# Performance work log

Measured on AMD Instinct MI355X. Metric: run time of the kernel, lower is better.

The kernel has to match this reference:

```python
import jax, jax.numpy as jnp
import numpy as np

B, T_SEQ, STATE, DIM_IN, DIM_K, DIM_V, LAYER = 8, 2048, 128, 1024, 64, 64, 4
T = T_SEQ + 2 * STATE  # 2304
LAMBDA_INIT = 0.8 - 0.6 * float(np.exp(-0.3 * LAYER))
NEG = -1e30


def setup_inputs() -> dict:
    key = jax.random.key(0)
    ks = jax.random.split(key, 20)
    def w(k, shape):
        return jax.random.normal(k, shape, dtype=jnp.float32) * 0.02
    inp = {"x": jax.random.normal(ks[0], (B, T, DIM_IN), dtype=jnp.float32)}
    # projection weights stored as (in, out) so y = x @ W
    inp["Wq"] = w(ks[1], (DIM_IN, 2 * DIM_K)); inp["Wk"] = w(ks[2], (DIM_IN, 2 * DIM_K)); inp["Wv"] = w(ks[3], (DIM_IN, 2 * DIM_V))
    inp["Wq_ss"] = w(ks[4], (DIM_IN, 2 * DIM_K)); inp["Wk_ss"] = w(ks[5], (DIM_IN, 2 * DIM_K)); inp["Wv_ss"] = w(ks[6], (DIM_IN, 2 * DIM_V))
    inp["Wq_se"] = w(ks[7], (DIM_IN, 2 * DIM_K)); inp["Wk_se"] = w(ks[8], (DIM_IN, 2 * DIM_K)); inp["Wv_se"] = w(ks[9], (DIM_IN, 2 * DIM_V))
    # layernorm params (torch defaults: ones/zeros)
    inp["g_in"] = jnp.ones((DIM_IN,), jnp.float32); inp["b_in"] = jnp.zeros((DIM_IN,), jnp.float32)
    inp["g_ss"] = jnp.ones((DIM_IN,), jnp.float32); inp["b_ss"] = jnp.zeros((DIM_IN,), jnp.float32)
    inp["g_se"] = jnp.ones((DIM_IN,), jnp.float32); inp["b_se"] = jnp.zeros((DIM_IN,), jnp.float32)
    inp["g_out"] = jnp.ones((2 * DIM_V,), jnp.float32); inp["b_out"] = jnp.zeros((2 * DIM_V,), jnp.float32)
    # lambda gate params
    inp["lq1"] = jax.random.normal(ks[10], (1, DIM_K), jnp.float32)
    inp["lq2"] = jax.random.normal(ks[11], (1, DIM_K), jnp.float32)
    inp["lk1"] = jax.random.normal(ks[12], (DIM_K, 1), jnp.float32)
    inp["lk2"] = jax.random.normal(ks[13], (DIM_K, 1), jnp.float32)
    return inp


def _ln(z, g, b, eps=1e-5):
    m = jnp.mean(z, axis=-1, keepdims=True)
    v = jnp.mean((z - m) ** 2, axis=-1, keepdims=True)
    return (z - m) * jax.lax.rsqrt(v + eps) * g + b


def reference(x, Wq, Wk, Wv, Wq_ss, Wk_ss, Wv_ss, Wq_se, Wk_se, Wv_se,
              g_in, b_in, g_ss, b_ss, g_se, b_se, g_out, b_out,
              lq1, lq2, lk1, lk2):
    # extract_state: split off state tokens at both ends
    xs, xm, xe = x[:, :STATE], x[:, STATE:-STATE], x[:, -STATE:]
    xm = _ln(xm, g_in, b_in)
    xs = _ln(xs, g_ss, b_ss)
    xe = _ln(xe, g_se, b_se)
    q = jnp.concatenate([xs @ Wq_ss, xm @ Wq, xe @ Wq_se], axis=1)  # (B,T,2K)
    k = jnp.concatenate([xs @ Wk_ss, xm @ Wk, xe @ Wk_se], axis=1)
    v = jnp.concatenate([xs @ Wv_ss, xm @ Wv, xe @ Wv_se], axis=1)  # (B,T,2V)
    q1, q2 = q[..., :DIM_K], q[..., DIM_K:]
    k1, k2 = k[..., :DIM_K], k[..., DIM_K:]
    scale = 1.0 / np.sqrt(DIM_K)
    t = q.shape[1]
    causal = jnp.triu(jnp.full((t, t), NEG, dtype=q.dtype), k=1)  # (T,T)
    s1 = jnp.einsum('btd,bsd->bts', q1, k1) * scale + causal
    s2 = jnp.einsum('btd,bsd->bts', q2, k2) * scale + causal
    a1 = jax.nn.softmax(s1, axis=-1)
    a2 = jax.nn.softmax(s2, axis=-1)
    o1 = jnp.einsum('bts,bsd->btd', a1, v)
    o2 = jnp.einsum('bts,bsd->btd', a2, v)
    lam = (jnp.exp(lq1 @ lk1) - jnp.exp(lq2 @ lk2))[0, 0] + LAMBDA_INIT
    att = o1 - lam * o2
    return _ln(att, g_out, b_out)
```

## Files before the change

### kernel.cpp

```cpp
#include <hip/hip_runtime.h>
#include <hip/hip_bf16.h>
#include <stdint.h>

#define B_ 8
#define T_ 2304
#define DIN 1024
#define LAMBDA_INIT_F 0.6192834728526788f

typedef __bf16 bf16x8 __attribute__((ext_vector_type(8)));
typedef float f32x4 __attribute__((ext_vector_type(4)));

__device__ __forceinline__ unsigned short f2bf(float f) {
    union { float f; unsigned int u; } v; v.f = f;
    unsigned int u = v.u;
    unsigned int r = (u + 0x7FFFu + ((u >> 16) & 1u)) >> 16;
    return (unsigned short)r;
}

__device__ __forceinline__ unsigned int pack2bf(float lo, float hi) {
    return ((unsigned int)f2bf(hi) << 16) | (unsigned int)f2bf(lo);
}

__global__ __launch_bounds__(256) void k_wtrans(
    const float* w0, const float* w1, const float* w2,
    const float* w3, const float* w4, const float* w5,
    const float* w6, const float* w7, const float* w8,
    unsigned short* __restrict__ wt)
{
    __shared__ float tile[64][65];
    int bx = blockIdx.x;
    int mat = bx >> 5;
    int tl = bx & 31;
    int tx = tl & 15;
    int ty = tl >> 4;
    const float* srcs[9] = {w0, w1, w2, w3, w4, w5, w6, w7, w8};
    const float* src = srcs[mat];
    int k0 = tx * 64, c0 = ty * 64;
    int t = threadIdx.x;
    int r = t >> 2, cg = (t & 3) << 4;
    const float* p = src + (size_t)(k0 + r) * 128 + c0 + cg;
#pragma unroll
    for (int i = 0; i < 4; ++i) {
        float4 v = *(const float4*)(p + i * 4);
        tile[r][cg + i * 4 + 0] = v.x;
        tile[r][cg + i * 4 + 1] = v.y;
        tile[r][cg + i * 4 + 2] = v.z;
        tile[r][cg + i * 4 + 3] = v.w;
    }
    __syncthreads();
    int seg = mat / 3, m = mat % 3;
    int crow = seg * 384 + m * 128 + c0 + r;
    unsigned short* dst = wt + (size_t)crow * 1024 + k0 + cg;
    __align__(16) unsigned short ob[16];
#pragma unroll
    for (int i = 0; i < 16; ++i) ob[i] = f2bf(tile[cg + i][r]);
    *(uint4*)(dst) = *(const uint4*)(ob);
    *(uint4*)(dst + 8) = *(const uint4*)(ob + 8);
}

__global__ __launch_bounds__(256) void k_ln(
    const float* __restrict__ x,
    const float* __restrict__ g_in, const float* __restrict__ b_in,
    const float* __restrict__ g_ss, const float* __restrict__ b_ss,
    const float* __restrict__ g_se, const float* __restrict__ b_se,
    unsigned short* __restrict__ xbf)
{
    int row = (blockIdx.x << 2) + (threadIdx.x >> 6);
    int l = threadIdx.x & 63;
    int t = row % T_;
    const float* gv; const float* bv;
    if (t < 128)       { gv = g_ss; bv = b_ss; }
    else if (t < 2176) { gv = g_in; bv = b_in; }
    else               { gv = g_se; bv = b_se; }
    const float* xp = x + (size_t)row * DIN + l * 4;
    float4 v0 = *(const float4*)(xp);
    float4 v1 = *(const float4*)(xp + 256);
    float4 v2 = *(const float4*)(xp + 512);
    float4 v3 = *(const float4*)(xp + 768);
    float s  = v0.x + v0.y + v0.z + v0.w + v1.x + v1.y + v1.z + v1.w
             + v2.x + v2.y + v2.z + v2.w + v3.x + v3.y + v3.z + v3.w;
    float s2 = v0.x*v0.x + v0.y*v0.y + v0.z*v0.z + v0.w*v0.w
             + v1.x*v1.x + v1.y*v1.y + v1.z*v1.z + v1.w*v1.w
             + v2.x*v2.x + v2.y*v2.y + v2.z*v2.z + v2.w*v2.w
             + v3.x*v3.x + v3.y*v3.y + v3.z*v3.z + v3.w*v3.w;
#pragma unroll
    for (int off = 1; off <= 32; off <<= 1) {
        s  += __shfl_xor(s,  off);
        s2 += __shfl_xor(s2, off);
    }
    float mean = s * (1.f / 1024.f);
    float rstd = rsqrtf(s2 * (1.f / 1024.f) - mean * mean + 1e-5f);
    unsigned short* op = xbf + (size_t)row * DIN + l * 4;
    const float* gp = gv + l * 4;
    const float* bp = bv + l * 4;
#pragma unroll
    for (int k = 0; k < 4; ++k) {
        float4 vv = (k == 0) ? v0 : (k == 1) ? v1 : (k == 2) ? v2 : v3;
        float4 gk = *(const float4*)(gp + k * 256);
        float4 bk = *(const float4*)(bp + k * 256);
        uint2 o;
        o.x = pack2bf((vv.x - mean) * rstd * gk.x + bk.x,
                      (vv.y - mean) * rstd * gk.y + bk.y);
        o.y = pack2bf((vv.z - mean) * rstd * gk.z + bk.z,
                      (vv.w - mean) * rstd * gk.w + bk.w);
        *(uint2*)(op + k * 256) = o;
    }
}

__global__ __launch_bounds__(512, 4) void k_proj2(
    const unsigned short* __restrict__ xbf,
    const unsigned short* __restrict__ wt,
    unsigned short* __restrict__ qo,
    unsigned short* __restrict__ ko,
    unsigned short* __restrict__ vto)
{
    __shared__ __align__(16) char smem[81920];

    int bid = blockIdx.x;
    int mt = bid >> 1, ch = bid & 1;
    int bb = mt / 18, tt = mt % 18;
    int seg = (tt == 0) ? 0 : ((tt < 17) ? 1 : 2);
    size_t arow0 = (size_t)mt * 128;
    int ncol0 = ch * 192;
    int wrow0 = seg * 384 + ncol0;

    int tid = threadIdx.x;
    int w = tid >> 6, l = tid & 63;
    int wr = w >> 2, wc = w & 3;
    int g4 = l >> 4, cr = l & 15;

    int rA0 = tid >> 3, cS = (tid & 7) << 4;
    const char* srcA0 = (const char*)xbf + (arow0 + rA0) * 2048 + cS;
    const char* srcA1 = srcA0 + (size_t)64 * 2048;
    int dA0 = rA0 * 128 + (cS ^ ((rA0 & 7) << 4));
    int dA1 = dA0 + 64 * 128;
    const char* srcW0 = (const char*)wt + (size_t)(wrow0 + rA0) * 2048 + cS;
    const char* srcW1 = srcW0 + (size_t)64 * 2048;
    const char* srcW2 = srcW0 + (size_t)128 * 2048;
    int dW0 = dA0, dW1 = dA0 + 64 * 128, dW2 = dA0 + 128 * 128;

    {
        uint4 a0 = *(const uint4*)srcA0;
        uint4 a1 = *(const uint4*)srcA1;
        uint4 w0 = *(const uint4*)srcW0;
        uint4 w1 = *(const uint4*)srcW1;
        uint4 w2 = *(const uint4*)srcW2;
        *(uint4*)(smem + dA0) = a0;
        *(uint4*)(smem + dA1) = a1;
        *(uint4*)(smem + 32768 + dW0) = w0;
        *(uint4*)(smem + 32768 + dW1) = w1;
        *(uint4*)(smem + 32768 + dW2) = w2;
    }
    __syncthreads();

    f32x4 acc[4][3] = {};
    for (int ks = 0; ks < 16; ++ks) {
        bool pf = (ks < 15);
        uint4 pa0, pa1, pw0, pw1, pw2;
        if (pf) {
            size_t o = (size_t)(ks + 1) * 128;
            pa0 = *(const uint4*)(srcA0 + o);
            pa1 = *(const uint4*)(srcA1 + o);
            pw0 = *(const uint4*)(srcW0 + o);
            pw1 = *(const uint4*)(srcW1 + o);
            pw2 = *(const uint4*)(srcW2 + o);
        }
        const char* Ab = smem + (ks & 1) * 16384;
        const char* Wb = smem + 32768 + (ks & 1) * 24576;
        __builtin_amdgcn_s_setprio(1);
#pragma unroll
        for (int kk = 0; kk < 2; ++kk) {
            int kb = kk * 64 + g4 * 16;
            bf16x8 af[4];
#pragma unroll
            for (int r4 = 0; r4 < 4; ++r4) {
                int rr = wr * 64 + r4 * 16 + cr;
                af[r4] = *(const bf16x8*)(Ab + rr * 128 + (kb ^ ((rr & 7) << 4)));
            }
            bf16x8 bfr[3];
#pragma unroll
            for (int nt = 0; nt < 3; ++nt) {
                int c = wc * 48 + nt * 16 + cr;
                bfr[nt] = *(const bf16x8*)(Wb + c * 128 + (kb ^ ((c & 7) << 4)));
            }
#pragma unroll
            for (int r4 = 0; r4 < 4; ++r4)
#pragma unroll
                for (int nt = 0; nt < 3; ++nt)
                    acc[r4][nt] = __builtin_amdgcn_mfma_f32_16x16x32_bf16(af[r4], bfr[nt], acc[r4][nt], 0, 0, 0);
        }
        __builtin_amdgcn_s_setprio(0);
        __syncthreads();
        if (pf) {
            char* An = smem + ((ks + 1) & 1) * 16384;
            char* Wn = smem + 32768 + ((ks + 1) & 1) * 24576;
            *(uint4*)(An + dA0) = pa0;
            *(uint4*)(An + dA1) = pa1;
            *(uint4*)(Wn + dW0) = pw0;
            *(uint4*)(Wn + dW1) = pw1;
            *(uint4*)(Wn + dW2) = pw2;
        }
        __syncthreads();
    }

#pragma unroll
    for (int r4 = 0; r4 < 4; ++r4) {
        size_t grow = arow0 + wr * 64 + r4 * 16 + g4 * 4;
#pragma unroll
        for (int nt = 0; nt < 3; ++nt) {
            int c = ncol0 + wc * 48 + nt * 16 + cr;
            f32x4 a = acc[r4][nt];
            if (c < 128) {
#pragma unroll
                for (int g = 0; g < 4; ++g)
                    qo[(grow + g) * 128 + c] = f2bf(a[g]);
            } else if (c < 256) {
#pragma unroll
                for (int g = 0; g < 4; ++g)
                    ko[(grow + g) * 128 + (c - 128)] = f2bf(a[g]);
            } else {
                int cv = c - 256;
                int trow = tt * 128 + wr * 64 + r4 * 16 + g4 * 4;
                uint2 o;
                o.x = pack2bf(a[0], a[1]);
                o.y = pack2bf(a[2], a[3]);
                *(uint2*)(vto + ((size_t)bb * 128 + cv) * T_ + trow) = o;
            }
        }
    }
}

__global__ __launch_bounds__(512, 2) void k_attn(
    const unsigned short* __restrict__ qp_,
    const unsigned short* __restrict__ kp_,
    const unsigned short* __restrict__ vp_,
    const float* __restrict__ lq1, const float* __restrict__ lq2,
    const float* __restrict__ lk1, const float* __restrict__ lk2,
    const float* __restrict__ g_out, const float* __restrict__ b_out,
    float* __restrict__ out)
{
    __shared__ __align__(16) char smem[69632];

    int bid = blockIdx.x;
    int j = 35 - (bid >> 3);
    int b = bid & 7;
    int t0 = j * 64;
    int tid = threadIdx.x;
    int w8 = tid >> 6;
    int qg = w8 & 3;
    int p  = w8 >> 2;
    int l = tid & 63;
    int g4 = l >> 4, q = l & 15;
    int q_g = t0 + qg * 16 + q;
    int grp = tid >> 8;
    int u = tid & 255;

    int rK = u >> 2, cK = (u & 3) << 6;
    const char* srcK0 = (const char*)(kp_ + ((size_t)b * T_ + rK) * 128) + cK;
    int rV = u >> 1, cV = (u & 1) << 6;
    const char* srcV0 = (const char*)(vp_ + ((size_t)b * 128 + rV) * T_) + cV;
    int swK = (rK & 7) << 4;
    char* KwB = smem + grp * 16384 + rK * 256;
    int oko0 = (cK +  0) ^ swK, oko1 = (cK + 16) ^ swK;
    int oko2 = (cK + 32) ^ swK, oko3 = (cK + 48) ^ swK;
    int swV = (rV & 7) << 4;
    char* VwB = smem + 32768 + grp * 16384 + rV * 128;
    int ovo0 = (cV +  0) ^ swV, ovo1 = (cV + 16) ^ swV;
    int ovo2 = (cV + 32) ^ swV, ovo3 = (cV + 48) ^ swV;

    bf16x8 qf[2][2];
#pragma unroll
    for (int br = 0; br < 2; ++br)
#pragma unroll
        for (int h = 0; h < 2; ++h)
            qf[br][h] = *(const bf16x8*)(qp_ + ((size_t)b * T_ + q_g) * 128 + br * 64 + h * 32 + g4 * 8);

    if (grp <= j) {
        const char* sK = srcK0 + (size_t)grp * 16384;
        uint4 ka0 = *(const uint4*)(sK);
        uint4 ka1 = *(const uint4*)(sK + 16);
        uint4 ka2 = *(const uint4*)(sK + 32);
        uint4 ka3 = *(const uint4*)(sK + 48);
        const char* sV = srcV0 + (size_t)grp * 128;
        uint4 va0 = *(const uint4*)(sV);
        uint4 va1 = *(const uint4*)(sV + 16);
        uint4 va2 = *(const uint4*)(sV + 32);
        uint4 va3 = *(const uint4*)(sV + 48);
        *(uint4*)(KwB + oko0) = ka0;
        *(uint4*)(KwB + oko1) = ka1;
        *(uint4*)(KwB + oko2) = ka2;
        *(uint4*)(KwB + oko3) = ka3;
        *(uint4*)(VwB + ovo0) = va0;
        *(uint4*)(VwB + ovo1) = va1;
        *(uint4*)(VwB + ovo2) = va2;
        *(uint4*)(VwB + ovo3) = va3;
    }
    __syncthreads();

    float mrun[2] = {-1e30f, -1e30f};
    float lrun[2] = {0.f, 0.f};
    f32x4 oacc[2][8] = {};
    const char* Kb = smem + p * 16384;
    const char* Vb = smem + 32768 + p * 16384;

    int nph = (j >> 1) + 1;
    for (int t = 0; t < nph; ++t) {
        int pf = 2 * (t + 1) + grp;
        bool pfv = (pf <= j);
        uint4 ka0, ka1, ka2, ka3, va0, va1, va2, va3;
        if (pfv) {
            const char* sK = srcK0 + (size_t)pf * 16384;
            ka0 = *(const uint4*)(sK);
            ka1 = *(const uint4*)(sK + 16);
            ka2 = *(const uint4*)(sK + 32);
            ka3 = *(const uint4*)(sK + 48);
            const char* sV = srcV0 + (size_t)pf * 128;
            va0 = *(const uint4*)(sV);
            va1 = *(const uint4*)(sV + 16);
            va2 = *(const uint4*)(sV + 32);
            va3 = *(const uint4*)(sV + 48);
        }

        int kt = 2 * t + p;
        if (kt <= j) {
            bool diag = (kt == j);
            unsigned int pk[2][4][2];
#pragma unroll
            for (int br = 0; br < 2; ++br) {
                f32x4 s[4] = {};
                __builtin_amdgcn_s_setprio(1);
#pragma unroll
                for (int h = 0; h < 2; ++h) {
#pragma unroll
                    for (int t4 = 0; t4 < 4; ++t4) {
                        int rk = t4 * 16 + q;
                        bf16x8 kf = *(const bf16x8*)(Kb + rk * 256 + ((br * 128 + h * 64 + g4 * 16) ^ ((rk & 7) << 4)));
                        s[t4] = __builtin_amdgcn_mfma_f32_16x16x32_bf16(kf, qf[br][h], s[t4], 0, 0, 0);
                    }
                }
                __builtin_amdgcn_s_setprio(0);
                float sv[16];
                float mx = -1e30f;
#pragma unroll
                for (int t4 = 0; t4 < 4; ++t4)
#pragma unroll
                    for (int r = 0; r < 4; ++r) {
                        float v = s[t4][r] * 0.125f;
                        if (diag) {
                            int kv_g = kt * 64 + t4 * 16 + g4 * 4 + r;
                            if (kv_g > q_g) v = -1e30f;
                        }
                        sv[t4 * 4 + r] = v;
                        mx = fmaxf(mx, v);
                    }
                mx = fmaxf(mx, __shfl_xor(mx, 16));
                mx = fmaxf(mx, __shfl_xor(mx, 32));
                float mn;
                if (__all(mx <= mrun[br] + 8.f)) {
                    mn = mrun[br];
                } else {
                    mn = fmaxf(mrun[br], mx);
                    float sf = __expf(mrun[br] - mn);
                    mrun[br] = mn;
                    lrun[br] *= sf;
#pragma unroll
                    for (int dblk = 0; dblk < 8; ++dblk)
#pragma unroll
                        for (int r = 0; r < 4; ++r)
                            oacc[br][dblk][r] *= sf;
                }
                float pr[16];
                float rs = 0.f;
#pragma unroll
                for (int i = 0; i < 16; ++i) {
                    pr[i] = __expf(sv[i] - mn);
                    rs += pr[i];
                }
                rs += __shfl_xor(rs, 16);
                rs += __shfl_xor(rs, 32);
                lrun[br] += rs;
#pragma unroll
                for (int t4 = 0; t4 < 4; ++t4) {
                    pk[br][t4][0] = pack2bf(pr[t4 * 4 + 0], pr[t4 * 4 + 1]);
                    pk[br][t4][1] = pack2bf(pr[t4 * 4 + 2], pr[t4 * 4 + 3]);
                }
            }
#pragma unroll
            for (int h = 0; h < 2; ++h) {
                bf16x8 pb[2];
                int s0 = q + (((g4 * 2) & 3) << 4);
                int s1 = q + (((g4 * 2 + 1) & 3) << 4);
                int sel = g4 >> 1;
#pragma unroll
                for (int br = 0; br < 2; ++br) {
                    unsigned int m0a = (unsigned int)__shfl((int)pk[br][2 * h][0], s0);
                    unsigned int m0b = (unsigned int)__shfl((int)pk[br][2 * h + 1][0], s0);
                    unsigned int m1a = (unsigned int)__shfl((int)pk[br][2 * h][1], s0);
                    unsigned int m1b = (unsigned int)__shfl((int)pk[br][2 * h + 1][1], s0);
                    unsigned int m2a = (unsigned int)__shfl((int)pk[br][2 * h][0], s1);
                    unsigned int m2b = (unsigned int)__shfl((int)pk[br][2 * h + 1][0], s1);
                    unsigned int m3a = (unsigned int)__shfl((int)pk[br][2 * h][1], s1);
                    unsigned int m3b = (unsigned int)__shfl((int)pk[br][2 * h + 1][1], s1);
                    union { unsigned int uu[4]; bf16x8 v; } pu;
                    pu.uu[0] = sel ? m0b : m0a;
                    pu.uu[1] = sel ? m1b : m1a;
                    pu.uu[2] = sel ? m2b : m2a;
                    pu.uu[3] = sel ? m3b : m3a;
                    pb[br] = pu.v;
                }
                __builtin_amdgcn_s_setprio(1);
#pragma unroll
                for (int dblk = 0; dblk < 8; ++dblk) {
                    int rv = dblk * 16 + q;
                    bf16x8 vf = *(const bf16x8*)(Vb + rv * 128 + ((h * 64 + g4 * 16) ^ ((rv & 7) << 4)));
                    oacc[0][dblk] = __builtin_amdgcn_mfma_f32_16x16x32_bf16(vf, pb[0], oacc[0][dblk], 0, 0, 0);
                    oacc[1][dblk] = __builtin_amdgcn_mfma_f32_16x16x32_bf16(vf, pb[1], oacc[1][dblk], 0, 0, 0);
                }
                __builtin_amdgcn_s_setprio(0);
            }
        }
        __syncthreads();
        if (pfv) {
            *(uint4*)(KwB + oko0) = ka0;
            *(uint4*)(KwB + oko1) = ka1;
            *(uint4*)(KwB + oko2) = ka2;
            *(uint4*)(KwB + oko3) = ka3;
            *(uint4*)(VwB + ovo0) = va0;
            *(uint4*)(VwB + ovo1) = va1;
            *(uint4*)(VwB + ovo2) = va2;
            *(uint4*)(VwB + ovo3) = va3;
        }
        __syncthreads();
    }

    float* Osh = (float*)smem;
    float* Msh = (float*)(smem + 65536);
    if (p == 1) {
        int base = qg * 4096 + l;
#pragma unroll
        for (int br = 0; br < 2; ++br)
#pragma unroll
            for (int dblk = 0; dblk < 8; ++dblk)
#pragma unroll
                for (int r = 0; r < 4; ++r)
                    Osh[base + (br * 32 + dblk * 4 + r) * 64] = oacc[br][dblk][r];
        float4 ml;
        ml.x = mrun[0]; ml.y = lrun[0]; ml.z = mrun[1]; ml.w = lrun[1];
        *(float4*)(Msh + (qg * 64 + l) * 4) = ml;
    }
    __syncthreads();
    if (p == 0) {
        float4 ml = *(const float4*)(Msh + (qg * 64 + l) * 4);
        float m1v[2] = {ml.x, ml.z}, l1v[2] = {ml.y, ml.w};
        float lfin[2], a0[2], a1[2];
#pragma unroll
        for (int br = 0; br < 2; ++br) {
            float mstar = fmaxf(mrun[br], m1v[br]);
            a0[br] = __expf(mrun[br] - mstar);
            a1[br] = __expf(m1v[br] - mstar);
            lfin[br] = a0[br] * lrun[br] + a1[br] * l1v[br];
        }
        int base = qg * 4096 + l;
#pragma unroll
        for (int br = 0; br < 2; ++br)
#pragma unroll
            for (int dblk = 0; dblk < 8; ++dblk)
#pragma unroll
                for (int r = 0; r < 4; ++r)
                    oacc[br][dblk][r] = a0[br] * oacc[br][dblk][r]
                        + a1[br] * Osh[base + (br * 32 + dblk * 4 + r) * 64];

        float pa = lq1[l] * lk1[l];
        float pb2 = lq2[l] * lk2[l];
#pragma unroll
        for (int off = 32; off >= 1; off >>= 1) {
            pa += __shfl_xor(pa, off);
            pb2 += __shfl_xor(pb2, off);
        }
        float lam = __expf(pa) - __expf(pb2) + LAMBDA_INIT_F;

        float att[8][4];
        float sm = 0.f;
        float inv1 = 1.f / lfin[0], inv2 = 1.f / lfin[1];
#pragma unroll
        for (int dblk = 0; dblk < 8; ++dblk)
#pragma unroll
            for (int r = 0; r < 4; ++r) {
                float a = oacc[0][dblk][r] * inv1 - lam * (oacc[1][dblk][r] * inv2);
                att[dblk][r] = a;
                sm += a;
            }
        sm += __shfl_xor(sm, 16);
        sm += __shfl_xor(sm, 32);
        float mean = sm * (1.f / 128.f);
        float sv2 = 0.f;
#pragma unroll
        for (int dblk = 0; dblk < 8; ++dblk)
#pragma unroll
            for (int r = 0; r < 4; ++r) {
                float d = att[dblk][r] - mean;
                sv2 += d * d;
            }
        sv2 += __shfl_xor(sv2, 16);
        sv2 += __shfl_xor(sv2, 32);
        float rstd = rsqrtf(sv2 * (1.f / 128.f) + 1e-5f);

        float* orow = out + ((size_t)b * T_ + q_g) * 128;
#pragma unroll
        for (int dblk = 0; dblk < 8; ++dblk) {
            int d0 = dblk * 16 + g4 * 4;
            float4 o;
            o.x = (att[dblk][0] - mean) * rstd * g_out[d0 + 0] + b_out[d0 + 0];
            o.y = (att[dblk][1] - mean) * rstd * g_out[d0 + 1] + b_out[d0 + 1];
            o.z = (att[dblk][2] - mean) * rstd * g_out[d0 + 2] + b_out[d0 + 2];
            o.w = (att[dblk][3] - mean) * rstd * g_out[d0 + 3] + b_out[d0 + 3];
            *(float4*)(orow + d0) = o;
        }
    }
}

extern "C" void kernel_launch(void* const* d_in, const int* in_sizes, int n_in,
                              void* d_out, int out_size, void* d_ws, size_t ws_size,
                              hipStream_t stream) {
    (void)in_sizes; (void)n_in; (void)out_size; (void)ws_size;
    const float* x = (const float*)d_in[0];
    char* ws = (char*)d_ws;
    unsigned short* wt  = (unsigned short*)ws;
    unsigned short* xbf = (unsigned short*)(ws + 2359296);
    unsigned short* qo  = (unsigned short*)(ws + 40108032);
    unsigned short* ko  = (unsigned short*)(ws + 44826624);
    unsigned short* vto = (unsigned short*)(ws + 49545216);

    hipLaunchKernelGGL(k_wtrans, dim3(288), dim3(256), 0, stream,
        (const float*)d_in[4], (const float*)d_in[5], (const float*)d_in[6],
        (const float*)d_in[1], (const float*)d_in[2], (const float*)d_in[3],
        (const float*)d_in[7], (const float*)d_in[8], (const float*)d_in[9], wt);

    hipLaunchKernelGGL(k_ln, dim3(4608), dim3(256), 0, stream,
        x,
        (const float*)d_in[10], (const float*)d_in[11],
        (const float*)d_in[12], (const float*)d_in[13],
        (const float*)d_in[14], (const float*)d_in[15],
        xbf);

    hipLaunchKernelGGL(k_proj2, dim3(288), dim3(512), 0, stream,
        xbf, wt, qo, ko, vto);

    hipLaunchKernelGGL(k_attn, dim3(288), dim3(512), 0, stream,
        qo, ko, vto,
        (const float*)d_in[18], (const float*)d_in[19],
        (const float*)d_in[20], (const float*)d_in[21],
        (const float*)d_in[16], (const float*)d_in[17],
        (float*)d_out);
}
```

Measured before the change: 131.2 us.

## Split long causal attention rows into KV chunks with a separate merge kernel

Query tiles with many causal KV tiles are split into up to three chunks of 12 KV tiles, so the attention grid grows from 288 to 576 blocks with more even work per block. Chunked tiles write bf16 partial outputs together with running max and sum to workspace, and a new merge kernel combines them, applies the lambda difference and the output layernorm. The cost is an extra kernel launch, extra global traffic for the partials, and bf16 rounding of the unnormalized partial accumulators. The partial buffers reuse the workspace region that held xbf.

```diff
diff --git a/kernel.cpp b/kernel.cpp
--- a/kernel.cpp
+++ b/kernel.cpp
@@ -19,6 +19,11 @@
 
 __device__ __forceinline__ unsigned int pack2bf(float lo, float hi) {
     return ((unsigned int)f2bf(hi) << 16) | (unsigned int)f2bf(lo);
+}
+
+__device__ __forceinline__ float bf2f(unsigned short u) {
+    union { unsigned int u; float f; } v; v.u = ((unsigned int)u) << 16;
+    return v.f;
 }
 
 __global__ __launch_bounds__(256) void k_wtrans(
@@ -237,14 +242,24 @@
     const float* __restrict__ lq1, const float* __restrict__ lq2,
     const float* __restrict__ lk1, const float* __restrict__ lk2,
     const float* __restrict__ g_out, const float* __restrict__ b_out,
+    unsigned short* __restrict__ opart,
+    float* __restrict__ mlpart,
     float* __restrict__ out)
 {
     __shared__ __align__(16) char smem[69632];
 
     int bid = blockIdx.x;
-    int j = 35 - (bid >> 3);
     int b = bid & 7;
+    int u = 71 - (bid >> 3);
+    int j, ci;
+    if (u < 12)      { j = u; ci = 0; }
+    else if (u < 36) { int v = u - 12; j = 12 + (v >> 1); ci = v & 1; }
+    else             { int v = u - 36; j = 24 + v / 3; ci = v % 3; }
+    int nch = (j + 12) / 12;
+    int c0 = ci * 12;
+    int ntile = min(12, j + 1 - c0);
     int t0 = j * 64;
+
     int tid = threadIdx.x;
     int w8 = tid >> 6;
     int qg = w8 & 3;
@@ -253,11 +268,11 @@
     int g4 = l >> 4, q = l & 15;
     int q_g = t0 + qg * 16 + q;
     int grp = tid >> 8;
-    int u = tid & 255;
-
-    int rK = u >> 2, cK = (u & 3) << 6;
+    int uu = tid & 255;
+
+    int rK = uu >> 2, cK = (uu & 3) << 6;
     const char* srcK0 = (const char*)(kp_ + ((size_t)b * T_ + rK) * 128) + cK;
-    int rV = u >> 1, cV = (u & 1) << 6;
+    int rV = uu >> 1, cV = (uu & 1) << 6;
     const char* srcV0 = (const char*)(vp_ + ((size_t)b * 128 + rV) * T_) + cV;
     int swK = (rK & 7) << 4;
     char* KwB = smem + grp * 16384 + rK * 256;
@@ -275,13 +290,13 @@
         for (int h = 0; h < 2; ++h)
             qf[br][h] = *(const bf16x8*)(qp_ + ((size_t)b * T_ + q_g) * 128 + br * 64 + h * 32 + g4 * 8);
 
-    if (grp <= j) {
-        const char* sK = srcK0 + (size_t)grp * 16384;
+    if (grp < ntile) {
+        const char* sK = srcK0 + (size_t)(c0 + grp) * 16384;
         uint4 ka0 = *(const uint4*)(sK);
         uint4 ka1 = *(const uint4*)(sK + 16);
         uint4 ka2 = *(const uint4*)(sK + 32);
         uint4 ka3 = *(const uint4*)(sK + 48);
-        const char* sV = srcV0 + (size_t)grp * 128;
+        const char* sV = srcV0 + (size_t)(c0 + grp) * 128;
         uint4 va0 = *(const uint4*)(sV);
         uint4 va1 = *(const uint4*)(sV + 16);
         uint4 va2 = *(const uint4*)(sV + 32);
@@ -303,26 +318,27 @@
     const char* Kb = smem + p * 16384;
     const char* Vb = smem + 32768 + p * 16384;
 
-    int nph = (j >> 1) + 1;
+    int nph = (ntile + 1) >> 1;
     for (int t = 0; t < nph; ++t) {
-        int pf = 2 * (t + 1) + grp;
-        bool pfv = (pf <= j);
+        int lpf = 2 * (t + 1) + grp;
+        bool pfv = (lpf < ntile);
         uint4 ka0, ka1, ka2, ka3, va0, va1, va2, va3;
         if (pfv) {
-            const char* sK = srcK0 + (size_t)pf * 16384;
+            const char* sK = srcK0 + (size_t)(c0 + lpf) * 16384;
             ka0 = *(const uint4*)(sK);
             ka1 = *(const uint4*)(sK + 16);
             ka2 = *(const uint4*)(sK + 32);
             ka3 = *(const uint4*)(sK + 48);
-            const char* sV = srcV0 + (size_t)pf * 128;
+            const char* sV = srcV0 + (size_t)(c0 + lpf) * 128;
             va0 = *(const uint4*)(sV);
             va1 = *(const uint4*)(sV + 16);
             va2 = *(const uint4*)(sV + 32);
             va3 = *(const uint4*)(sV + 48);
         }
 
-        int kt = 2 * t + p;
-        if (kt <= j) {
+        int lt = 2 * t + p;
+        if (lt < ntile) {
+            int kt = c0 + lt;
             bool diag = (kt == j);
             unsigned int pk[2][4][2];
 #pragma unroll
@@ -401,11 +417,11 @@
                     unsigned int m2b = (unsigned int)__shfl((int)pk[br][2 * h + 1][0], s1);
                     unsigned int m3a = (unsigned int)__shfl((int)pk[br][2 * h][1], s1);
                     unsigned int m3b = (unsigned int)__shfl((int)pk[br][2 * h + 1][1], s1);
-                    union { unsigned int uu[4]; bf16x8 v; } pu;
-                    pu.uu[0] = sel ? m0b : m0a;
-                    pu.uu[1] = sel ? m1b : m1a;
-                    pu.uu[2] = sel ? m2b : m2a;
-                    pu.uu[3] = sel ? m3b : m3a;
+                    union { unsigned int uv[4]; bf16x8 v; } pu;
+                    pu.uv[0] = sel ? m0b : m0a;
+                    pu.uv[1] = sel ? m1b : m1a;
+                    pu.uv[2] = sel ? m2b : m2a;
+                    pu.uv[3] = sel ? m3b : m3a;
                     pb[br] = pu.v;
                 }
                 __builtin_amdgcn_s_setprio(1);
@@ -452,70 +468,189 @@
     if (p == 0) {
         float4 ml = *(const float4*)(Msh + (qg * 64 + l) * 4);
         float m1v[2] = {ml.x, ml.z}, l1v[2] = {ml.y, ml.w};
-        float lfin[2], a0[2], a1[2];
+        float lfin[2], mst[2];
 #pragma unroll
         for (int br = 0; br < 2; ++br) {
             float mstar = fmaxf(mrun[br], m1v[br]);
-            a0[br] = __expf(mrun[br] - mstar);
-            a1[br] = __expf(m1v[br] - mstar);
-            lfin[br] = a0[br] * lrun[br] + a1[br] * l1v[br];
-        }
-        int base = qg * 4096 + l;
-#pragma unroll
-        for (int br = 0; br < 2; ++br)
+            float a0 = __expf(mrun[br] - mstar);
+            float a1 = __expf(m1v[br] - mstar);
+            lfin[br] = a0 * lrun[br] + a1 * l1v[br];
+            mst[br] = mstar;
+            int base = qg * 4096 + l;
 #pragma unroll
             for (int dblk = 0; dblk < 8; ++dblk)
 #pragma unroll
                 for (int r = 0; r < 4; ++r)
-                    oacc[br][dblk][r] = a0[br] * oacc[br][dblk][r]
-                        + a1[br] * Osh[base + (br * 32 + dblk * 4 + r) * 64];
-
-        float pa = lq1[l] * lk1[l];
-        float pb2 = lq2[l] * lk2[l];
-#pragma unroll
-        for (int off = 32; off >= 1; off >>= 1) {
-            pa += __shfl_xor(pa, off);
-            pb2 += __shfl_xor(pb2, off);
-        }
-        float lam = __expf(pa) - __expf(pb2) + LAMBDA_INIT_F;
-
-        float att[8][4];
-        float sm = 0.f;
-        float inv1 = 1.f / lfin[0], inv2 = 1.f / lfin[1];
-#pragma unroll
-        for (int dblk = 0; dblk < 8; ++dblk)
-#pragma unroll
-            for (int r = 0; r < 4; ++r) {
-                float a = oacc[0][dblk][r] * inv1 - lam * (oacc[1][dblk][r] * inv2);
-                att[dblk][r] = a;
-                sm += a;
-            }
-        sm += __shfl_xor(sm, 16);
-        sm += __shfl_xor(sm, 32);
-        float mean = sm * (1.f / 128.f);
-        float sv2 = 0.f;
-#pragma unroll
-        for (int dblk = 0; dblk < 8; ++dblk)
-#pragma unroll
-            for (int r = 0; r < 4; ++r) {
-                float d = att[dblk][r] - mean;
-                sv2 += d * d;
-            }
-        sv2 += __shfl_xor(sv2, 16);
-        sv2 += __shfl_xor(sv2, 32);
-        float rstd = rsqrtf(sv2 * (1.f / 128.f) + 1e-5f);
-
-        float* orow = out + ((size_t)b * T_ + q_g) * 128;
-#pragma unroll
-        for (int dblk = 0; dblk < 8; ++dblk) {
-            int d0 = dblk * 16 + g4 * 4;
-            float4 o;
-            o.x = (att[dblk][0] - mean) * rstd * g_out[d0 + 0] + b_out[d0 + 0];
-            o.y = (att[dblk][1] - mean) * rstd * g_out[d0 + 1] + b_out[d0 + 1];
-            o.z = (att[dblk][2] - mean) * rstd * g_out[d0 + 2] + b_out[d0 + 2];
-            o.w = (att[dblk][3] - mean) * rstd * g_out[d0 + 3] + b_out[d0 + 3];
-            *(float4*)(orow + d0) = o;
-        }
+                    oacc[br][dblk][r] = a0 * oacc[br][dblk][r]
+                        + a1 * Osh[base + (br * 32 + dblk * 4 + r) * 64];
+        }
+
+        int row = qg * 16 + q;
+        if (nch == 1) {
+            float pa = lq1[l] * lk1[l];
+            float pb2 = lq2[l] * lk2[l];
+#pragma unroll
+            for (int off = 32; off >= 1; off >>= 1) {
+                pa += __shfl_xor(pa, off);
+                pb2 += __shfl_xor(pb2, off);
+            }
+            float lam = __expf(pa) - __expf(pb2) + LAMBDA_INIT_F;
+
+            float att[8][4];
+            float sm = 0.f;
+            float inv1 = 1.f / lfin[0], inv2 = 1.f / lfin[1];
+#pragma unroll
+            for (int dblk = 0; dblk < 8; ++dblk)
+#pragma unroll
+                for (int r = 0; r < 4; ++r) {
+                    float a = oacc[0][dblk][r] * inv1 - lam * (oacc[1][dblk][r] * inv2);
+                    att[dblk][r] = a;
+                    sm += a;
+                }
+            sm += __shfl_xor(sm, 16);
+            sm += __shfl_xor(sm, 32);
+            float mean = sm * (1.f / 128.f);
+            float sv2 = 0.f;
+#pragma unroll
+            for (int dblk = 0; dblk < 8; ++dblk)
+#pragma unroll
+                for (int r = 0; r < 4; ++r) {
+                    float d = att[dblk][r] - mean;
+                    sv2 += d * d;
+                }
+            sv2 += __shfl_xor(sv2, 16);
+            sv2 += __shfl_xor(sv2, 32);
+            float rstd = rsqrtf(sv2 * (1.f / 128.f) + 1e-5f);
+
+            float* orow = out + ((size_t)b * T_ + q_g) * 128;
+#pragma unroll
+            for (int dblk = 0; dblk < 8; ++dblk) {
+                int d0 = dblk * 16 + g4 * 4;
+                float4 o;
+                o.x = (att[dblk][0] - mean) * rstd * g_out[d0 + 0] + b_out[d0 + 0];
+                o.y = (att[dblk][1] - mean) * rstd * g_out[d0 + 1] + b_out[d0 + 1];
+                o.z = (att[dblk][2] - mean) * rstd * g_out[d0 + 2] + b_out[d0 + 2];
+                o.w = (att[dblk][3] - mean) * rstd * g_out[d0 + 3] + b_out[d0 + 3];
+                *(float4*)(orow + d0) = o;
+            }
+        } else {
+            int slot = (b * 36 + j) * 3 + ci;
+            char* ob = (char*)opart + (size_t)slot * 32768;
+#pragma unroll
+            for (int br = 0; br < 2; ++br) {
+#pragma unroll
+                for (int dblk = 0; dblk < 8; ++dblk) {
+                    uint2 o;
+                    o.x = pack2bf(oacc[br][dblk][0], oacc[br][dblk][1]);
+                    o.y = pack2bf(oacc[br][dblk][2], oacc[br][dblk][3]);
+                    *(uint2*)(ob + br * 16384 + row * 256 + (dblk * 16 + g4 * 4) * 2) = o;
+                }
+                float2 mlv;
+                mlv.x = mst[br];
+                mlv.y = lfin[br];
+                *(float2*)(mlpart + ((size_t)slot * 128 + br * 64 + row) * 2) = mlv;
+            }
+        }
+    }
+}
+
+__global__ __launch_bounds__(512) void k_merge(
+    const unsigned short* __restrict__ opart,
+    const float* __restrict__ mlpart,
+    const float* __restrict__ lq1, const float* __restrict__ lq2,
+    const float* __restrict__ lk1, const float* __restrict__ lk2,
+    const float* __restrict__ g_out, const float* __restrict__ b_out,
+    float* __restrict__ out)
+{
+    int bid = blockIdx.x;
+    int b = bid & 7;
+    int j = 12 + (bid >> 3);
+    int nch = (j + 12) / 12;
+    int tid = threadIdx.x;
+    int row = tid >> 3;
+    int d0 = (tid & 7) * 16;
+    int l = tid & 63;
+
+    float pa = lq1[l] * lk1[l];
+    float pb = lq2[l] * lk2[l];
+#pragma unroll
+    for (int off = 32; off >= 1; off >>= 1) {
+        pa += __shfl_xor(pa, off);
+        pb += __shfl_xor(pb, off);
+    }
+    float lam = __expf(pa) - __expf(pb) + LAMBDA_INIT_F;
+
+    int slotb = (b * 36 + j) * 3;
+    float res[2][16];
+#pragma unroll
+    for (int br = 0; br < 2; ++br) {
+        float m0 = mlpart[((size_t)(slotb + 0) * 128 + br * 64 + row) * 2];
+        float l0 = mlpart[((size_t)(slotb + 0) * 128 + br * 64 + row) * 2 + 1];
+        float m1 = mlpart[((size_t)(slotb + 1) * 128 + br * 64 + row) * 2];
+        float l1 = mlpart[((size_t)(slotb + 1) * 128 + br * 64 + row) * 2 + 1];
+        float m2 = -1e30f, l2 = 0.f;
+        if (nch == 3) {
+            m2 = mlpart[((size_t)(slotb + 2) * 128 + br * 64 + row) * 2];
+            l2 = mlpart[((size_t)(slotb + 2) * 128 + br * 64 + row) * 2 + 1];
+        }
+        float mstar = fmaxf(fmaxf(m0, m1), m2);
+        float w0 = __expf(m0 - mstar);
+        float w1 = __expf(m1 - mstar);
+        float w2 = (nch == 3) ? __expf(m2 - mstar) : 0.f;
+        float lsum = w0 * l0 + w1 * l1 + w2 * l2;
+
+        float acc[16] = {};
+#pragma unroll
+        for (int c = 0; c < 3; ++c) {
+            if (c >= nch) break;
+            float wc = (c == 0) ? w0 : (c == 1) ? w1 : w2;
+            const char* ob = (const char*)opart + (size_t)(slotb + c) * 32768
+                           + br * 16384 + row * 256 + d0 * 2;
+            uint4 v0 = *(const uint4*)(ob);
+            uint4 v1 = *(const uint4*)(ob + 16);
+            const unsigned int vv[8] = {v0.x, v0.y, v0.z, v0.w, v1.x, v1.y, v1.z, v1.w};
+#pragma unroll
+            for (int i = 0; i < 8; ++i) {
+                acc[i * 2]     += wc * bf2f((unsigned short)(vv[i] & 0xFFFF));
+                acc[i * 2 + 1] += wc * bf2f((unsigned short)(vv[i] >> 16));
+            }
+        }
+        float inv = 1.f / lsum;
+#pragma unroll
+        for (int i = 0; i < 16; ++i) res[br][i] = acc[i] * inv;
+    }
+
+    float att[16];
+    float sm = 0.f;
+#pragma unroll
+    for (int i = 0; i < 16; ++i) {
+        att[i] = res[0][i] - lam * res[1][i];
+        sm += att[i];
+    }
+    sm += __shfl_xor(sm, 1);
+    sm += __shfl_xor(sm, 2);
+    sm += __shfl_xor(sm, 4);
+    float mean = sm * (1.f / 128.f);
+    float sv2 = 0.f;
+#pragma unroll
+    for (int i = 0; i < 16; ++i) {
+        float d = att[i] - mean;
+        sv2 += d * d;
+    }
+    sv2 += __shfl_xor(sv2, 1);
+    sv2 += __shfl_xor(sv2, 2);
+    sv2 += __shfl_xor(sv2, 4);
+    float rstd = rsqrtf(sv2 * (1.f / 128.f) + 1e-5f);
+
+    float* orow = out + ((size_t)b * T_ + j * 64 + row) * 128 + d0;
+#pragma unroll
+    for (int k = 0; k < 4; ++k) {
+        float4 o;
+        o.x = (att[k * 4 + 0] - mean) * rstd * g_out[d0 + k * 4 + 0] + b_out[d0 + k * 4 + 0];
+        o.y = (att[k * 4 + 1] - mean) * rstd * g_out[d0 + k * 4 + 1] + b_out[d0 + k * 4 + 1];
+        o.z = (att[k * 4 + 2] - mean) * rstd * g_out[d0 + k * 4 + 2] + b_out[d0 + k * 4 + 2];
+        o.w = (att[k * 4 + 3] - mean) * rstd * g_out[d0 + k * 4 + 3] + b_out[d0 + k * 4 + 3];
+        *(float4*)(orow + k * 4) = o;
     }
 }
 
@@ -530,6 +665,8 @@
     unsigned short* qo  = (unsigned short*)(ws + 40108032);
     unsigned short* ko  = (unsigned short*)(ws + 44826624);
     unsigned short* vto = (unsigned short*)(ws + 49545216);
+    unsigned short* opart = (unsigned short*)(ws + 2359296);
+    float*          mlpart = (float*)(ws + 2359296 + 28311552);
 
     hipLaunchKernelGGL(k_wtrans, dim3(288), dim3(256), 0, stream,
         (const float*)d_in[4], (const float*)d_in[5], (const float*)d_in[6],
@@ -546,10 +683,18 @@
     hipLaunchKernelGGL(k_proj2, dim3(288), dim3(512), 0, stream,
         xbf, wt, qo, ko, vto);
 
-    hipLaunchKernelGGL(k_attn, dim3(288), dim3(512), 0, stream,
+    hipLaunchKernelGGL(k_attn, dim3(576), dim3(512), 0, stream,
         qo, ko, vto,
         (const float*)d_in[18], (const float*)d_in[19],
         (const float*)d_in[20], (const float*)d_in[21],
         (const float*)d_in[16], (const float*)d_in[17],
+        opart, mlpart,
         (float*)d_out);
-}
+
+    hipLaunchKernelGGL(k_merge, dim3(192), dim3(512), 0, stream,
+        opart, mlpart,
+        (const float*)d_in[18], (const float*)d_in[19],
+        (const float*)d_in[20], (const float*)d_in[21],
+        (const float*)d_in[16], (const float*)d_in[17],
+        (float*)d_out);
+}
```

Result: faster. 128.1 us (-2.3%).
